# Kernel optimization log

Hardware: AMD Instinct MI355X
Metric: run time of the kernel (lower is better)

Reference implementation:

```python
import jax, jax.numpy as jnp
import numpy as np

N, B, C, T, IN_DIM, L, RANK, OUT_DIM = 2000, 16, 32, 12, 2, 3, 4, 1
CN = C // 4  # channel_num = 8
EPS = 1e-5


def _adj_month():
    a = np.diag(np.ones(12)) / 3.0
    np.fill_diagonal(a[1:], 1.0 / 3.0)
    np.fill_diagonal(a[:, 1:], 1.0 / 3.0)
    a[0, 11] = 1.0 / 3.0
    a[11, 0] = 1.0 / 3.0
    return jnp.asarray(a, dtype=jnp.float32)


def _circ_conv(xb, w, b, k):
    # xb: [B,N,C,T]; w: [N,CN,C,k]; b: [N,CN]  ->  [B,N,CN,T]
    # Circular pad on the right by k-1 (matches F.pad(...,(0,k-1)) mode='circular').
    Tt = xb.shape[-1]
    xp = jnp.concatenate([xb, xb[..., :k - 1]], axis=-1)          # [B,N,C,T+k-1]
    win = jnp.stack([xp[..., j:j + Tt] for j in range(k)], axis=-1)  # [B,N,C,T,k]
    return jnp.einsum('bnctk,nock->bnot', win, w) + b[None, :, :, None]


def setup_inputs() -> dict:
    key = jax.random.key(0)
    ks = jax.random.split(key, 32)

    def rn(i, shape, scale=0.05):
        return jax.random.normal(ks[i], shape, dtype=jnp.float32) * scale

    D_cw = CN * C * 18 * L   # 13824
    D_cb = CN * 4 * L        # 96
    D_rw = C * C * L         # 3072
    D_rb = C * L             # 96

    inp = jax.random.normal(ks[0], (B, IN_DIM, N, T + 1), dtype=jnp.float32)
    inp = inp.at[0, 0, 0, -1].set(5.0)  # valid month index
    adj = jax.random.uniform(ks[1], (N, N), dtype=jnp.float32) / N

    return dict(
        input=inp, adj=adj,
        characteristics=rn(2, (N, 12, RANK), 0.5),
        W_convw=rn(3, (RANK, D_cw)), b_convw=rn(4, (D_cw,)),
        W_convb=rn(5, (RANK, D_cb)), b_convb=rn(6, (D_cb,)),
        W_gatew=rn(7, (RANK, D_cw)), b_gatew=rn(8, (D_cw,)),
        W_gateb=rn(9, (RANK, D_cb)), b_gateb=rn(10, (D_cb,)),
        W_resw=rn(11, (RANK, D_rw)), b_resw=rn(12, (D_rw,)),
        W_resb=rn(13, (RANK, D_rb)), b_resb=rn(14, (D_rb,)),
        start_w=rn(15, (C, IN_DIM), 0.5), start_b=rn(16, (C,)),
        skip0_w=rn(17, (C, IN_DIM, T), 0.2), skip0_b=rn(18, (C,)),
        skip_w=rn(19, (L, C, T), 0.2), skip_b=rn(20, (L, C)),
        skipE_w=rn(21, (C, T), 0.2), skipE_b=rn(22, (C,)),
        ln_w=jnp.ones((L, C, N, T), jnp.float32),
        ln_b=jnp.zeros((L, C, N, T), jnp.float32),
        end1_w=rn(23, (C, C), 0.2), end1_b=rn(24, (C,)),
        end2_w=rn(25, (OUT_DIM, C), 0.2), end2_b=rn(26, (OUT_DIM,)),
    )


def reference(input, adj, characteristics, W_convw, b_convw, W_convb, b_convb,
              W_gatew, b_gatew, W_gateb, b_gateb, W_resw, b_resw, W_resb, b_resb,
              start_w, start_b, skip0_w, skip0_b, skip_w, skip_b, skipE_w, skipE_b,
              ln_w, ln_b, end1_w, end1_b, end2_w, end2_b):
    # month index from last time slot (eval mode: dropout = identity)
    month = jnp.mod(input[0, 0, 0, -1].astype(jnp.int32), 12)
    x_in = input[..., :T]                                   # [B,IN,N,T]

    am = _adj_month()                                       # [12,12]
    char = jnp.einsum('ms,nsr->nmr', am, characteristics)   # [N,12,R]
    char_m = jnp.take(char, month, axis=1)                  # [N,R]
    ch = adj @ char_m                                       # graph aggregation [N,R]

    cw_all = ch @ W_convw + b_convw                         # [N, CN*C*18*L]
    cb_all = ch @ W_convb + b_convb                         # [N, CN*4*L]
    gw_all = ch @ W_gatew + b_gatew
    gb_all = ch @ W_gateb + b_gateb
    rw_all = ch @ W_resw + b_resw                           # [N, C*C*L]
    rb_all = ch @ W_resb + b_resb                           # [N, C*L]

    x = jnp.einsum('bint,ci->bcnt', x_in, start_w) + start_b[None, :, None, None]
    skip = jnp.einsum('bint,cit->bcn', x_in, skip0_w) + skip0_b[None, :, None]  # [B,C,N]

    pw = CN * C                                             # 256
    # (kernel slice lo, hi, width) per multiscale branch
    slices = [(0, 2, 2), (2, 5, 3), (5, 11, 6), (11, 18, 7)]
    q = N * CN

    for i in range(L):
        residual = x
        cw = cw_all[:, i * 18 * pw:(i + 1) * 18 * pw].reshape(N, CN, C, 18)
        gw = gw_all[:, i * 18 * pw:(i + 1) * 18 * pw].reshape(N, CN, C, 18)
        # NOTE: torch flattens bias node-major THEN slices quarters -> reproduces
        # the original (node-mixing) bias indexing exactly.
        cb_flat = cb_all[:, i * 4 * CN:(i + 1) * 4 * CN].reshape(-1)   # [N*4*CN]
        gb_flat = gb_all[:, i * 4 * CN:(i + 1) * 4 * CN].reshape(-1)

        xb = jnp.transpose(x, (0, 2, 1, 3))                 # [B,N,C,T]
        f_segs, g_segs = [], []
        for s, (lo, hi, k) in enumerate(slices):
            f = _circ_conv(xb, cw[..., lo:hi], cb_flat[s * q:(s + 1) * q].reshape(N, CN), k)
            g = _circ_conv(xb, gw[..., lo:hi], gb_flat[s * q:(s + 1) * q].reshape(N, CN), k)
            f_segs.append(jnp.transpose(f, (0, 2, 1, 3)))   # [B,CN,N,T]
            g_segs.append(jnp.transpose(g, (0, 2, 1, 3)))
        filt = jnp.tanh(jnp.concatenate(f_segs, axis=1))    # [B,C,N,T]
        gate = jax.nn.sigmoid(jnp.concatenate(g_segs, axis=1))
        x = filt * gate

        s_out = jnp.einsum('bcnt,ct->bcn', x, skip_w[i]) + skip_b[i][None, :, None]
        skip = s_out + skip

        rw = rw_all[:, i * C * C:(i + 1) * C * C].reshape(N, C, C)   # [N,out,in]
        rb = rb_all[:, i * C:(i + 1) * C]                            # [N,C]
        xr = jnp.einsum('bnct,noc->bnot', jnp.transpose(x, (0, 2, 1, 3)), rw) \
             + rb[None, :, :, None]
        x = jnp.transpose(xr, (0, 2, 1, 3)) + residual

        # LayerNorm over all non-batch dims (C,N,T) with affine params
        mu = jnp.mean(x, axis=(1, 2, 3), keepdims=True)
        var = jnp.mean(jnp.square(x - mu), axis=(1, 2, 3), keepdims=True)
        x = (x - mu) / jnp.sqrt(var + EPS) * ln_w[i][None] + ln_b[i][None]

    sE = jnp.einsum('bcnt,ct->bcn', x, skipE_w) + skipE_b[None, :, None]
    skip = jax.nn.relu(sE + skip)                           # [B,C,N]
    y = jax.nn.relu(jnp.einsum('bcn,oc->bon', skip, end1_w) + end1_b[None, :, None])
    y = jnp.einsum('bcn,oc->bon', y, end2_w) + end2_b[None, :, None]
    return y[..., None]                                     # [B,OUT_DIM,N,1]
```

## Files before the change

### kernel.cpp

```cpp
#include <hip/hip_runtime.h>

#define NN 2000
#define TT 12

#define XOFF    0
#define SKOFF   6144000
#define CHOFF   7168000
#define CMOFF   7176000
#define STOFF   7184000
#define PARTOFF 7184100
#define PKWOFF  7248100
#define PKBOFF  7358692
#define PKROFF  7386340

typedef __fp16 f16x8 __attribute__((ext_vector_type(8)));
typedef float  f32x4 __attribute__((ext_vector_type(4)));

union U32H2 { unsigned int u; __fp16 h[2]; };
__device__ __forceinline__ unsigned int pkh(float a, float b){
  U32H2 v; v.h[0] = (__fp16)a; v.h[1] = (__fp16)b; return v.u;
}
__device__ __forceinline__ float fsig(float x){ return 1.0f/(1.0f + __expf(-x)); }
__device__ __forceinline__ float ftanh(float x){ return 1.0f - 2.0f/(1.0f + __expf(2.0f*x)); }

__global__ void k_charm(const float* __restrict__ input,
                        const float* __restrict__ charac,
                        float* __restrict__ cm)
{
  int idx = blockIdx.x*256 + threadIdx.x;
  if (idx >= NN*4) return;
  int n = idx >> 2, r = idx & 3;
  int mv = (int)input[TT];
  int m = ((mv % 12) + 12) % 12;
  int m0 = (m + 11) % 12, m2 = (m + 1) % 12;
  const float* base = charac + n*48;
  cm[idx] = (base[m0*4+r] + base[m*4+r] + base[m2*4+r]) * (1.0f/3.0f);
}

__global__ __launch_bounds__(256) void k_ch(const float* __restrict__ adj,
                                            const float* __restrict__ cm,
                                            float* __restrict__ ch)
{
  __shared__ float red[256][4];
  int n = blockIdx.x, t = threadIdx.x;
  float s0=0.f, s1=0.f, s2=0.f, s3=0.f;
  const float* arow = adj + (size_t)n*NN;
  for (int c = t; c < NN; c += 256){
    float a = arow[c];
    float4 v = *reinterpret_cast<const float4*>(cm + c*4);
    s0 = fmaf(a, v.x, s0); s1 = fmaf(a, v.y, s1);
    s2 = fmaf(a, v.z, s2); s3 = fmaf(a, v.w, s3);
  }
  red[t][0]=s0; red[t][1]=s1; red[t][2]=s2; red[t][3]=s3;
  __syncthreads();
  for (int off = 128; off > 0; off >>= 1){
    if (t < off){
      red[t][0]+=red[t+off][0]; red[t][1]+=red[t+off][1];
      red[t][2]+=red[t+off][2]; red[t][3]+=red[t+off][3];
    }
    __syncthreads();
  }
  if (t < 4) ch[n*4+t] = red[0][t];
}

__global__ __launch_bounds__(256) void k_prep(
    const float* __restrict__ Wcw, const float* __restrict__ bcw,
    const float* __restrict__ Wgw, const float* __restrict__ bgw,
    const float* __restrict__ Wrw, const float* __restrict__ brw,
    float* __restrict__ PKW, float* __restrict__ PKB, float* __restrict__ PKR)
{
  int col = blockIdx.x*256 + threadIdx.x;
  if (col < 13824){
    int layer = col / 4608;
    int i     = col - layer*4608;
    int o     = i / 576;
    int rem   = i - o*576;
    int c     = rem / 18;
    int u     = rem - c*18;
    size_t j  = (size_t)layer*4608 + o*576 + u*32 + c;
    float4 a = make_float4(Wcw[col], Wcw[13824+col], Wcw[27648+col], Wcw[41472+col]);
    float4 b = make_float4(Wgw[col], Wgw[13824+col], Wgw[27648+col], Wgw[41472+col]);
    *reinterpret_cast<float4*>(PKW + j*8)     = a;
    *reinterpret_cast<float4*>(PKW + j*8 + 4) = b;
    *reinterpret_cast<float2*>(PKB + j*2) = make_float2(bcw[col], bgw[col]);
  }
  if (col < 3072){
    float4 r = make_float4(Wrw[col], Wrw[3072+col], Wrw[6144+col], Wrw[9216+col]);
    *reinterpret_cast<float4*>(PKR + (size_t)col*8) = r;
    PKR[(size_t)col*8 + 4] = brw[col];
  }
}

__global__ __launch_bounds__(256) void k_stats(
    int layer, const float* __restrict__ parts, float* __restrict__ stats)
{
  __shared__ float red[256];
  const int j = blockIdx.x, tid = threadIdx.x;
  float s = 0.f;
  for (int i = tid; i < NN; i += 256) s += parts[(size_t)i*32 + j];
  red[tid] = s;
  __syncthreads();
  for (int off = 128; off > 0; off >>= 1){
    if (tid < off) red[tid] += red[tid+off];
    __syncthreads();
  }
  if (tid == 0) stats[layer*32 + j] = red[0];
}

__global__ __launch_bounds__(256,3) void k_layer(
    int layer,
    __fp16* __restrict__ xbuf, float* __restrict__ skipbuf,
    const float* __restrict__ ch, const float* __restrict__ stats,
    float* __restrict__ parts,
    const float* __restrict__ input,
    const float* __restrict__ PKW, const float* __restrict__ PKB,
    const float* __restrict__ PKR,
    const float* __restrict__ Wcb, const float* __restrict__ bcb,
    const float* __restrict__ Wgb, const float* __restrict__ bgb,
    const float* __restrict__ Wrb, const float* __restrict__ brb,
    const float* __restrict__ start_w, const float* __restrict__ start_b,
    const float* __restrict__ sk0w, const float* __restrict__ sk0b,
    const float* __restrict__ skw_all, const float* __restrict__ skb_all,
    const float* __restrict__ lnw_all, const float* __restrict__ lnb_all)
{
  __shared__ __fp16 AhG[10752];
  __shared__ __fp16 xh[7680];
  __shared__ __fp16 rwh[1280];
  __shared__ float skred[1024];
  __shared__ float wred[128];
  __shared__ float ubuf[1280];
  __shared__ float skwv[384];
  __shared__ float skbv[32], fbias[32], gbias[32], rbv[32];
  __shared__ float muv[16], rsv[16];

  const int tid = threadIdx.x;
  const int n = blockIdx.x;

  float* swv  = ubuf;
  float* sbv  = ubuf + 64;
  float* s0wv = ubuf + 96;
  float* s0bv = ubuf + 864;
  float* xin  = ubuf + 896;
  float* lnwv = ubuf;
  float* lnbv = ubuf + 384;

  const float c0v = ch[n*4+0], c1v = ch[n*4+1], c2v = ch[n*4+2], c3v = ch[n*4+3];

  for (int i = tid; i < 32; i += 256) skbv[i] = skb_all[layer*32+i];
  for (int i = tid; i < 384; i += 256) skwv[i] = skw_all[layer*384+i];
  if (layer == 0){
    for (int i = tid; i < 64; i += 256) swv[i] = start_w[i];
    for (int i = tid; i < 32; i += 256){ sbv[i] = start_b[i]; s0bv[i] = sk0b[i]; }
    for (int i = tid; i < 768; i += 256) s0wv[i] = sk0w[i];
    for (int i = tid; i < 384; i += 256){
      int bb = i/24, r = i%24, d = r/12, t = r%12;
      xin[i] = input[(((size_t)bb*2 + d)*NN + n)*13 + t];
    }
  } else {
    for (int i = tid; i < 384; i += 256){
      int c = i/12, t = i%12;
      size_t o = (((size_t)(layer-1)*32 + c)*NN + n)*12 + t;
      lnwv[i] = lnw_all[o]; lnbv[i] = lnb_all[o];
    }
    if (tid < 16){
      float S1 = stats[(layer-1)*32 + tid];
      float S2 = stats[(layer-1)*32 + 16 + tid];
      const float M = 768000.0f;
      float mu = S1 / M;
      muv[tid] = mu;
      rsv[tid] = rsqrtf(S2/M - mu*mu + 1e-5f);
    }
  }

  {
    const int cc = tid & 31;
    int g2 = tid >> 5;
    const float* pkwL = PKW + (size_t)layer*4608*8;
    const float* pkbL = PKB + (size_t)layer*4608*2;
#pragma unroll
    for (int it = 0; it < 18; ++it, g2 += 8){
      int o  = g2 / 18;
      int u  = g2 - o*18;
      int s  = (u >= 2) + (u >= 5) + (u >= 11);
      int lo = (s == 0) ? 0 : ((s == 1) ? 2 : ((s == 2) ? 5 : 11));
      int jj = u - lo;
      size_t j = (size_t)g2*32 + cc;
      float4 pwf = *reinterpret_cast<const float4*>(pkwL + j*8);
      float4 pwg = *reinterpret_cast<const float4*>(pkwL + j*8 + 4);
      float2 pb  = *reinterpret_cast<const float2*>(pkbL + j*2);
      float wf = fmaf(c0v, pwf.x, fmaf(c1v, pwf.y,
                 fmaf(c2v, pwf.z, fmaf(c3v, pwf.w, pb.x))));
      float wg = fmaf(c0v, pwg.x, fmaf(c1v, pwg.y,
                 fmaf(c2v, pwg.z, fmaf(c3v, pwg.w, pb.y))));
      int base = (s >= 2) ? 3328 : 0;
      int strd = (s >= 2) ? 232 : 104;
      int r    = ((s & 1) << 3) + o;
      int k    = jj*32 + cc;
      AhG[base + r*strd + k]        = (__fp16)wf;
      AhG[base + (16 + r)*strd + k] = (__fp16)wg;
    }
  }
  for (int i = tid; i < 1024; i += 256){
    int grp = i >> 8, rem = i & 255, r = rem >> 5, c = rem & 31;
    int base = (grp < 2) ? 0 : 3328;
    int strd = (grp < 2) ? 104 : 232;
    int off  = (grp < 2) ? 64 : 192;
    int gofs = (grp & 1) ? 16*strd : 0;
    AhG[base + gofs + r*strd + off + c] = (__fp16)0.f;
  }
  for (int i = tid; i < 1024; i += 256){
    int col = layer*1024 + i;
    float4 pr = *reinterpret_cast<const float4*>(PKR + (size_t)col*8);
    float rb = PKR[(size_t)col*8 + 4];
    float v = fmaf(c0v, pr.x, fmaf(c1v, pr.y,
              fmaf(c2v, pr.z, fmaf(c3v, pr.w, rb))));
    rwh[(i>>5)*40 + (i&31)] = (__fp16)v;
  }
  if (tid < 32){
    int oc = tid;
    int s = oc >> 3;
    int v = ((n&3)<<3) + (oc&7);
    int col = layer*32 + v;
    float cb0 = ch[(s*500 + (n>>2))*4 + 0];
    float cb1 = ch[(s*500 + (n>>2))*4 + 1];
    float cb2 = ch[(s*500 + (n>>2))*4 + 2];
    float cb3 = ch[(s*500 + (n>>2))*4 + 3];
    fbias[oc] = fmaf(cb0, Wcb[col], fmaf(cb1, Wcb[96+col],
                fmaf(cb2, Wcb[192+col], fmaf(cb3, Wcb[288+col], bcb[col]))));
    gbias[oc] = fmaf(cb0, Wgb[col], fmaf(cb1, Wgb[96+col],
                fmaf(cb2, Wgb[192+col], fmaf(cb3, Wgb[288+col], bgb[col]))));
    int colr = layer*32 + oc;
    rbv[oc] = fmaf(c0v, Wrb[colr], fmaf(c1v, Wrb[96+colr],
              fmaf(c2v, Wrb[192+colr], fmaf(c3v, Wrb[288+colr], brb[colr]))));
  }
  __syncthreads();

  if (tid < 192){
    int b = tid & 15, t = tid >> 4;
    float xv[32];
    if (layer == 0){
      float xa = xin[b*24 + t], xb2 = xin[b*24 + 12 + t];
#pragma unroll
      for (int c = 0; c < 32; ++c)
        xv[c] = fmaf(swv[c*2], xa, fmaf(swv[c*2+1], xb2, sbv[c]));
    } else {
      const uint4* src = reinterpret_cast<const uint4*>(
          xbuf + (((size_t)b*NN + n)*12 + t)*32);
      uint4 u0 = src[0], u1 = src[1], u2 = src[2], u3 = src[3];
      unsigned int uu[16] = {u0.x,u0.y,u0.z,u0.w, u1.x,u1.y,u1.z,u1.w,
                             u2.x,u2.y,u2.z,u2.w, u3.x,u3.y,u3.z,u3.w};
      float mu = muv[b], rs = rsv[b];
#pragma unroll
      for (int j = 0; j < 16; ++j){
        U32H2 vv; vv.u = uu[j];
        int c = j*2;
        xv[c]   = fmaf(((float)vv.h[0]-mu)*rs, lnwv[c*12+t],     lnbv[c*12+t]);
        xv[c+1] = fmaf(((float)vv.h[1]-mu)*rs, lnwv[(c+1)*12+t], lnbv[(c+1)*12+t]);
      }
    }
    unsigned int pk[16];
#pragma unroll
    for (int j = 0; j < 16; ++j) pk[j] = pkh(xv[2*j], xv[2*j+1]);
    uint4* dst = reinterpret_cast<uint4*>(&xh[(t*16 + b)*40]);
    dst[0] = make_uint4(pk[0], pk[1], pk[2], pk[3]);
    dst[1] = make_uint4(pk[4], pk[5], pk[6], pk[7]);
    dst[2] = make_uint4(pk[8], pk[9], pk[10], pk[11]);
    dst[3] = make_uint4(pk[12],pk[13],pk[14],pk[15]);
  }
  __syncthreads();

  const int lane = tid & 63, w = tid >> 6;
  const int h = w & 1, nh = w >> 1;
  const int r16 = lane & 15, hi4 = lane >> 4;
  const int c0 = hi4*8;
  const int oc0 = h*16 + hi4*4;

  const __fp16* Ab = AhG + (h ? 3328 : 0);
  const int As  = h ? 232 : 104;
  const int njj = h ? 7 : 3;
  f16x8 aF[7], aG[7];
#pragma unroll 7
  for (int jj = 0; jj < 7; ++jj) if (jj < njj){
    aF[jj] = *reinterpret_cast<const f16x8*>(&Ab[r16*As + jj*32 + c0]);
    aG[jj] = *reinterpret_cast<const f16x8*>(&Ab[(16 + r16)*As + jj*32 + c0]);
  }
  f16x8 ar = *reinterpret_cast<const f16x8*>(&rwh[(h*16 + r16)*40 + c0]);
  float fb4[4], gb4[4], rb4[4];
#pragma unroll
  for (int i2 = 0; i2 < 4; ++i2){
    fb4[i2] = fbias[oc0+i2]; gb4[i2] = gbias[oc0+i2]; rb4[i2] = rbv[oc0+i2];
  }
  __syncthreads();
  __fp16* gh = AhG;

  float sv[4] = {0.f, 0.f, 0.f, 0.f};
#pragma unroll
  for (int q = 0; q < 6; ++q){
    int nt = nh*6 + q;
    f32x4 accf = {0.f,0.f,0.f,0.f}, accg = {0.f,0.f,0.f,0.f};
#pragma unroll 7
    for (int jj = 0; jj < 7; ++jj) if (jj < njj){
      int tp = nt + jj; if (tp >= 12) tp -= 12;
      f16x8 bf = *reinterpret_cast<const f16x8*>(&xh[(tp*16 + r16)*40 + c0]);
      accf = __builtin_amdgcn_mfma_f32_16x16x32_f16(aF[jj], bf, accf, 0, 0, 0);
      accg = __builtin_amdgcn_mfma_f32_16x16x32_f16(aG[jj], bf, accg, 0, 0, 0);
    }
    float gv4[4];
#pragma unroll
    for (int i2 = 0; i2 < 4; ++i2){
      float fv = ftanh(accf[i2] + fb4[i2]);
      float gg = fsig(accg[i2] + gb4[i2]);
      gv4[i2] = fv * gg;
      sv[i2] = fmaf(gv4[i2], skwv[(oc0+i2)*12 + nt], sv[i2]);
    }
    *reinterpret_cast<uint2*>(&gh[(nt*16 + r16)*40 + oc0]) =
        make_uint2(pkh(gv4[0], gv4[1]), pkh(gv4[2], gv4[3]));
  }
#pragma unroll
  for (int i2 = 0; i2 < 4; ++i2)
    skred[((oc0+i2)*16 + r16)*2 + nh] = sv[i2];
  __syncthreads();

  for (int e = tid; e < 512; e += 256){
    int b = e >> 5, oc = e & 31;
    float sk = skred[(oc*16+b)*2] + skred[(oc*16+b)*2+1] + skbv[oc];
    size_t so = ((size_t)b*NN + n)*32 + oc;
    if (layer == 0){
      float s0 = s0bv[oc];
#pragma unroll
      for (int r = 0; r < 24; ++r) s0 = fmaf(xin[b*24+r], s0wv[oc*24+r], s0);
      skipbuf[so] = sk + s0;
    } else {
      skipbuf[so] += sk;
    }
  }
  {
    float s1 = 0.f, s2 = 0.f;
#pragma unroll
    for (int q = 0; q < 6; ++q){
      int nt = nh*6 + q;
      f16x8 bg = *reinterpret_cast<const f16x8*>(&gh[(nt*16 + r16)*40 + c0]);
      f32x4 z = {0.f,0.f,0.f,0.f};
      f32x4 acc = __builtin_amdgcn_mfma_f32_16x16x32_f16(ar, bg, z, 0, 0, 0);
      uint2 xu = *reinterpret_cast<const uint2*>(&xh[(nt*16 + r16)*40 + oc0]);
      U32H2 ua, ub; ua.u = xu.x; ub.u = xu.y;
      float o0 = acc[0] + rb4[0] + (float)ua.h[0];
      float o1 = acc[1] + rb4[1] + (float)ua.h[1];
      float o2 = acc[2] + rb4[2] + (float)ub.h[0];
      float o3 = acc[3] + rb4[3] + (float)ub.h[1];
      *reinterpret_cast<uint2*>(
          xbuf + (((size_t)r16*NN + n)*12 + nt)*32 + oc0) =
          make_uint2(pkh(o0, o1), pkh(o2, o3));
      s1 += o0 + o1 + o2 + o3;
      s2 = fmaf(o0,o0, fmaf(o1,o1, fmaf(o2,o2, fmaf(o3,o3, s2))));
    }
    s1 += __shfl_xor(s1, 16); s2 += __shfl_xor(s2, 16);
    s1 += __shfl_xor(s1, 32); s2 += __shfl_xor(s2, 32);
    if (hi4 == 0){
      wred[(w*16 + r16)*2]     = s1;
      wred[(w*16 + r16)*2 + 1] = s2;
    }
  }
  __syncthreads();
  if (tid < 16){
    float a1 = 0.f, a2 = 0.f;
    for (int w2 = 0; w2 < 4; ++w2){
      a1 += wred[(w2*16 + tid)*2];
      a2 += wred[(w2*16 + tid)*2 + 1];
    }
    parts[(size_t)n*32 + tid]      = a1;
    parts[(size_t)n*32 + 16 + tid] = a2;
  }
}

__global__ __launch_bounds__(256) void k_final(
    const __fp16* __restrict__ xbuf, const float* __restrict__ skipbuf,
    const float* __restrict__ stats,
    const float* __restrict__ lnw_all, const float* __restrict__ lnb_all,
    const float* __restrict__ skEw, const float* __restrict__ skEb,
    const float* __restrict__ e1w, const float* __restrict__ e1b,
    const float* __restrict__ e2w, const float* __restrict__ e2b,
    float* __restrict__ out)
{
  __shared__ float lnw[384], lnb[384], skE[384];
  __shared__ float e1[32*33];
  __shared__ float e1bv[32], e2v[32], skEbv[32];
  __shared__ float muv[16], rsv[16];
  __shared__ float skf[8][33];
  const int tid = threadIdx.x, n = blockIdx.x;
  for (int i = tid; i < 384; i += 256){
    int c = i/12, t = i%12;
    size_t o = (((size_t)2*32 + c)*NN + n)*12 + t;
    lnw[i] = lnw_all[o]; lnb[i] = lnb_all[o];
    skE[i] = skEw[i];
  }
  for (int i = tid; i < 1024; i += 256) e1[(i>>5)*33 + (i&31)] = e1w[i];
  if (tid < 32){ e1bv[tid] = e1b[tid]; e2v[tid] = e2w[tid]; skEbv[tid] = skEb[tid]; }
  if (tid < 16){
    float S1 = stats[64+tid], S2 = stats[80+tid];
    const float M = 768000.0f;
    float mu = S1/M; muv[tid] = mu;
    rsv[tid] = rsqrtf(S2/M - mu*mu + 1e-5f);
  }
  __syncthreads();
  const float e2b0 = e2b[0];
  for (int bo = 0; bo < 2; ++bo){
    const int g = tid >> 5, c = tid & 31, b = bo*8 + g;
    float xr[12];
#pragma unroll
    for (int t = 0; t < 12; ++t)
      xr[t] = (float)xbuf[(((size_t)b*NN + n)*12 + t)*32 + c];
    const float mu = muv[b], rs = rsv[b];
    float se = 0.0f;
#pragma unroll
    for (int t = 0; t < 12; ++t){
      float xv = fmaf((xr[t]-mu)*rs, lnw[c*12+t], lnb[c*12+t]);
      se = fmaf(xv, skE[c*12+t], se);
    }
    float sk = se + skEbv[c] + skipbuf[((size_t)b*NN+n)*32 + c];
    skf[g][c] = fmaxf(sk, 0.0f);
    __syncthreads();
    float acc = e1bv[c];
#pragma unroll
    for (int cc = 0; cc < 32; ++cc) acc = fmaf(skf[g][cc], e1[c*33+cc], acc);
    float y1 = fmaxf(acc, 0.0f);
    float part = y1 * e2v[c];
#pragma unroll
    for (int off = 16; off > 0; off >>= 1) part += __shfl_down(part, off, 32);
    if (c == 0) out[(size_t)b*NN + n] = part + e2b0;
    __syncthreads();
  }
}

extern "C" void kernel_launch(void* const* d_in, const int* in_sizes, int n_in,
                              void* d_out, int out_size, void* d_ws, size_t ws_size,
                              hipStream_t stream)
{
  (void)in_sizes; (void)n_in; (void)out_size; (void)ws_size;
  const float* input   = (const float*)d_in[0];
  const float* adj     = (const float*)d_in[1];
  const float* charac  = (const float*)d_in[2];
  const float* Wcw     = (const float*)d_in[3];
  const float* bcw     = (const float*)d_in[4];
  const float* Wcb     = (const float*)d_in[5];
  const float* bcb     = (const float*)d_in[6];
  const float* Wgw     = (const float*)d_in[7];
  const float* bgw     = (const float*)d_in[8];
  const float* Wgb     = (const float*)d_in[9];
  const float* bgb     = (const float*)d_in[10];
  const float* Wrw     = (const float*)d_in[11];
  const float* brw     = (const float*)d_in[12];
  const float* Wrb     = (const float*)d_in[13];
  const float* brb     = (const float*)d_in[14];
  const float* start_w = (const float*)d_in[15];
  const float* start_b = (const float*)d_in[16];
  const float* sk0w    = (const float*)d_in[17];
  const float* sk0b    = (const float*)d_in[18];
  const float* skw     = (const float*)d_in[19];
  const float* skb     = (const float*)d_in[20];
  const float* skEw    = (const float*)d_in[21];
  const float* skEb    = (const float*)d_in[22];
  const float* lnw     = (const float*)d_in[23];
  const float* lnb     = (const float*)d_in[24];
  const float* e1w     = (const float*)d_in[25];
  const float* e1b     = (const float*)d_in[26];
  const float* e2w     = (const float*)d_in[27];
  const float* e2b     = (const float*)d_in[28];

  float* ws     = (float*)d_ws;
  __fp16* xbuf  = (__fp16*)(ws + XOFF);
  float* skipb  = ws + SKOFF;
  float* chbuf  = ws + CHOFF;
  float* cmbuf  = ws + CMOFF;
  float* stats  = ws + STOFF;
  float* parts  = ws + PARTOFF;
  float* PKW    = ws + PKWOFF;
  float* PKB    = ws + PKBOFF;
  float* PKR    = ws + PKROFF;
  float* outp   = (float*)d_out;

  k_prep<<<54, 256, 0, stream>>>(Wcw, bcw, Wgw, bgw, Wrw, brw, PKW, PKB, PKR);
  k_charm<<<32, 256, 0, stream>>>(input, charac, cmbuf);
  k_ch<<<NN, 256, 0, stream>>>(adj, cmbuf, chbuf);
  for (int layer = 0; layer < 3; ++layer){
    k_layer<<<NN, 256, 0, stream>>>(layer, xbuf, skipb, chbuf, stats, parts, input,
        PKW, PKB, PKR, Wcb, bcb, Wgb, bgb, Wrb, brb,
        start_w, start_b, sk0w, sk0b, skw, skb, lnw, lnb);
    k_stats<<<32, 256, 0, stream>>>(layer, parts, stats);
  }
  k_final<<<NN, 256, 0, stream>>>(xbuf, skipb, stats, lnw, lnb,
      skEw, skEb, e1w, e1b, e2w, e2b, outp);
}
```

Baseline: 218.9 us.

## Fuse month-averaging into k_ch, prefetch xbuf early, specialize MFMA loops per half

Removes the k_charm kernel and computes the three-month averaged characteristics inline inside k_ch, saving a launch and an intermediate buffer at the cost of redundant reads of charac per row. In k_layer, the previous-layer activations are loaded into registers at kernel start so their latency overlaps parameter staging, with the barrier moved earlier to match. The conv MFMA loops are split into fully unrolled branches for the 3-tap and 7-tap halves instead of a guarded loop. This raises register pressure.

```diff
diff --git a/kernel.cpp b/kernel.cpp
--- a/kernel.cpp
+++ b/kernel.cpp
@@ -23,33 +23,30 @@
 __device__ __forceinline__ float fsig(float x){ return 1.0f/(1.0f + __expf(-x)); }
 __device__ __forceinline__ float ftanh(float x){ return 1.0f - 2.0f/(1.0f + __expf(2.0f*x)); }
 
-__global__ void k_charm(const float* __restrict__ input,
-                        const float* __restrict__ charac,
-                        float* __restrict__ cm)
-{
-  int idx = blockIdx.x*256 + threadIdx.x;
-  if (idx >= NN*4) return;
-  int n = idx >> 2, r = idx & 3;
-  int mv = (int)input[TT];
-  int m = ((mv % 12) + 12) % 12;
-  int m0 = (m + 11) % 12, m2 = (m + 1) % 12;
-  const float* base = charac + n*48;
-  cm[idx] = (base[m0*4+r] + base[m*4+r] + base[m2*4+r]) * (1.0f/3.0f);
-}
-
 __global__ __launch_bounds__(256) void k_ch(const float* __restrict__ adj,
-                                            const float* __restrict__ cm,
+                                            const float* __restrict__ input,
+                                            const float* __restrict__ charac,
                                             float* __restrict__ ch)
 {
   __shared__ float red[256][4];
   int n = blockIdx.x, t = threadIdx.x;
+  int mv = (int)input[TT];
+  int m = ((mv % 12) + 12) % 12;
+  int m0 = (m + 11) % 12, m2 = (m + 1) % 12;
   float s0=0.f, s1=0.f, s2=0.f, s3=0.f;
   const float* arow = adj + (size_t)n*NN;
   for (int c = t; c < NN; c += 256){
     float a = arow[c];
-    float4 v = *reinterpret_cast<const float4*>(cm + c*4);
-    s0 = fmaf(a, v.x, s0); s1 = fmaf(a, v.y, s1);
-    s2 = fmaf(a, v.z, s2); s3 = fmaf(a, v.w, s3);
+    const float* cb = charac + c*48;
+    float4 v0 = *reinterpret_cast<const float4*>(cb + m0*4);
+    float4 v1 = *reinterpret_cast<const float4*>(cb + m*4);
+    float4 v2 = *reinterpret_cast<const float4*>(cb + m2*4);
+    float vx = (v0.x + v1.x + v2.x) * (1.0f/3.0f);
+    float vy = (v0.y + v1.y + v2.y) * (1.0f/3.0f);
+    float vz = (v0.z + v1.z + v2.z) * (1.0f/3.0f);
+    float vw = (v0.w + v1.w + v2.w) * (1.0f/3.0f);
+    s0 = fmaf(a, vx, s0); s1 = fmaf(a, vy, s1);
+    s2 = fmaf(a, vz, s2); s3 = fmaf(a, vw, s3);
   }
   red[t][0]=s0; red[t][1]=s1; red[t][2]=s2; red[t][3]=s3;
   __syncthreads();
@@ -146,6 +143,14 @@
 
   const float c0v = ch[n*4+0], c1v = ch[n*4+1], c2v = ch[n*4+2], c3v = ch[n*4+3];
 
+  uint4 pre0 = {0,0,0,0}, pre1 = {0,0,0,0}, pre2 = {0,0,0,0}, pre3 = {0,0,0,0};
+  if (layer > 0 && tid < 192){
+    int b = tid & 15, t = tid >> 4;
+    const uint4* src = reinterpret_cast<const uint4*>(
+        xbuf + (((size_t)b*NN + n)*12 + t)*32);
+    pre0 = src[0]; pre1 = src[1]; pre2 = src[2]; pre3 = src[3];
+  }
+
   for (int i = tid; i < 32; i += 256) skbv[i] = skb_all[layer*32+i];
   for (int i = tid; i < 384; i += 256) skwv[i] = skw_all[layer*384+i];
   if (layer == 0){
@@ -171,6 +176,7 @@
       rsv[tid] = rsqrtf(S2/M - mu*mu + 1e-5f);
     }
   }
+  __syncthreads();
 
   {
     const int cc = tid & 31;
@@ -233,8 +239,6 @@
     rbv[oc] = fmaf(c0v, Wrb[colr], fmaf(c1v, Wrb[96+colr],
               fmaf(c2v, Wrb[192+colr], fmaf(c3v, Wrb[288+colr], brb[colr]))));
   }
-  __syncthreads();
-
   if (tid < 192){
     int b = tid & 15, t = tid >> 4;
     float xv[32];
@@ -244,11 +248,8 @@
       for (int c = 0; c < 32; ++c)
         xv[c] = fmaf(swv[c*2], xa, fmaf(swv[c*2+1], xb2, sbv[c]));
     } else {
-      const uint4* src = reinterpret_cast<const uint4*>(
-          xbuf + (((size_t)b*NN + n)*12 + t)*32);
-      uint4 u0 = src[0], u1 = src[1], u2 = src[2], u3 = src[3];
-      unsigned int uu[16] = {u0.x,u0.y,u0.z,u0.w, u1.x,u1.y,u1.z,u1.w,
-                             u2.x,u2.y,u2.z,u2.w, u3.x,u3.y,u3.z,u3.w};
+      unsigned int uu[16] = {pre0.x,pre0.y,pre0.z,pre0.w, pre1.x,pre1.y,pre1.z,pre1.w,
+                             pre2.x,pre2.y,pre2.z,pre2.w, pre3.x,pre3.y,pre3.z,pre3.w};
       float mu = muv[b], rs = rsv[b];
 #pragma unroll
       for (int j = 0; j < 16; ++j){
@@ -275,14 +276,20 @@
   const int c0 = hi4*8;
   const int oc0 = h*16 + hi4*4;
 
-  const __fp16* Ab = AhG + (h ? 3328 : 0);
-  const int As  = h ? 232 : 104;
-  const int njj = h ? 7 : 3;
   f16x8 aF[7], aG[7];
-#pragma unroll 7
-  for (int jj = 0; jj < 7; ++jj) if (jj < njj){
-    aF[jj] = *reinterpret_cast<const f16x8*>(&Ab[r16*As + jj*32 + c0]);
-    aG[jj] = *reinterpret_cast<const f16x8*>(&Ab[(16 + r16)*As + jj*32 + c0]);
+  if (h){
+    const __fp16* Ab = AhG + 3328;
+#pragma unroll
+    for (int jj = 0; jj < 7; ++jj){
+      aF[jj] = *reinterpret_cast<const f16x8*>(&Ab[r16*232 + jj*32 + c0]);
+      aG[jj] = *reinterpret_cast<const f16x8*>(&Ab[(16 + r16)*232 + jj*32 + c0]);
+    }
+  } else {
+#pragma unroll
+    for (int jj = 0; jj < 3; ++jj){
+      aF[jj] = *reinterpret_cast<const f16x8*>(&AhG[r16*104 + jj*32 + c0]);
+      aG[jj] = *reinterpret_cast<const f16x8*>(&AhG[(16 + r16)*104 + jj*32 + c0]);
+    }
   }
   f16x8 ar = *reinterpret_cast<const f16x8*>(&rwh[(h*16 + r16)*40 + c0]);
   float fb4[4], gb4[4], rb4[4];
@@ -298,12 +305,22 @@
   for (int q = 0; q < 6; ++q){
     int nt = nh*6 + q;
     f32x4 accf = {0.f,0.f,0.f,0.f}, accg = {0.f,0.f,0.f,0.f};
-#pragma unroll 7
-    for (int jj = 0; jj < 7; ++jj) if (jj < njj){
-      int tp = nt + jj; if (tp >= 12) tp -= 12;
-      f16x8 bf = *reinterpret_cast<const f16x8*>(&xh[(tp*16 + r16)*40 + c0]);
-      accf = __builtin_amdgcn_mfma_f32_16x16x32_f16(aF[jj], bf, accf, 0, 0, 0);
-      accg = __builtin_amdgcn_mfma_f32_16x16x32_f16(aG[jj], bf, accg, 0, 0, 0);
+    if (h){
+#pragma unroll
+      for (int jj = 0; jj < 7; ++jj){
+        int tp = nt + jj; if (tp >= 12) tp -= 12;
+        f16x8 bf = *reinterpret_cast<const f16x8*>(&xh[(tp*16 + r16)*40 + c0]);
+        accf = __builtin_amdgcn_mfma_f32_16x16x32_f16(aF[jj], bf, accf, 0, 0, 0);
+        accg = __builtin_amdgcn_mfma_f32_16x16x32_f16(aG[jj], bf, accg, 0, 0, 0);
+      }
+    } else {
+#pragma unroll
+      for (int jj = 0; jj < 3; ++jj){
+        int tp = nt + jj; if (tp >= 12) tp -= 12;
+        f16x8 bf = *reinterpret_cast<const f16x8*>(&xh[(tp*16 + r16)*40 + c0]);
+        accf = __builtin_amdgcn_mfma_f32_16x16x32_f16(aF[jj], bf, accf, 0, 0, 0);
+        accg = __builtin_amdgcn_mfma_f32_16x16x32_f16(aG[jj], bf, accg, 0, 0, 0);
+      }
     }
     float gv4[4];
 #pragma unroll
@@ -471,7 +488,6 @@
   __fp16* xbuf  = (__fp16*)(ws + XOFF);
   float* skipb  = ws + SKOFF;
   float* chbuf  = ws + CHOFF;
-  float* cmbuf  = ws + CMOFF;
   float* stats  = ws + STOFF;
   float* parts  = ws + PARTOFF;
   float* PKW    = ws + PKWOFF;
@@ -480,8 +496,7 @@
   float* outp   = (float*)d_out;
 
   k_prep<<<54, 256, 0, stream>>>(Wcw, bcw, Wgw, bgw, Wrw, brw, PKW, PKB, PKR);
-  k_charm<<<32, 256, 0, stream>>>(input, charac, cmbuf);
-  k_ch<<<NN, 256, 0, stream>>>(adj, cmbuf, chbuf);
+  k_ch<<<NN, 256, 0, stream>>>(adj, input, charac, chbuf);
   for (int layer = 0; layer < 3; ++layer){
     k_layer<<<NN, 256, 0, stream>>>(layer, xbuf, skipb, chbuf, stats, parts, input,
         PKW, PKB, PKR, Wcb, bcb, Wgb, bgb, Wrb, brb,
```

Measured after the change: 238.3 us. 1.09x slower.
